# Kernel optimization log

Measured on AMD Instinct MI355X. Metric: run time of the kernel, lower is better.

Reference implementation:

```python
import jax, jax.numpy as jnp
import numpy as np

D_MODEL = 1024
STATE_DIM = 64
SEQ_L = 2048


def hippo_legs_A(N):
    n = jnp.arange(N, dtype=jnp.float32)
    two_n1 = 2.0 * n + 1.0
    sq = jnp.sqrt(two_n1[:, None] * two_n1[None, :])
    A = jnp.tril(sq, k=-1) * -1.0
    return A + jnp.diag(-(n + 1.0))


def setup_inputs() -> dict:
    key = jax.random.key(0)
    kB, kC = jax.random.split(key)
    N = STATE_DIM
    n = jnp.arange(N, dtype=jnp.float32)
    B_ref = jnp.sqrt(2.0 * n + 1.0)  # (N,)
    B = jnp.tile(B_ref[None, :], (D_MODEL, 1)) + 0.01 * jax.random.normal(kB, (D_MODEL, N), dtype=jnp.float32)
    C = 0.1 * jax.random.normal(kC, (D_MODEL, N), dtype=jnp.float32)
    D = jnp.zeros((D_MODEL,), dtype=jnp.float32)
    log_dt = jnp.log(jnp.asarray(0.1, dtype=jnp.float32))
    return {"B": B, "C": C, "D": D, "log_dt": log_dt, "L": SEQ_L}


def reference(B, C, D, log_dt, L):
    N = B.shape[1]
    A = hippo_legs_A(N)                       # (N,N) continuous-time HiPPO-LegS
    dt = jax.nn.softplus(log_dt) + 1e-06
    I = jnp.eye(N, dtype=A.dtype)
    lhs = I - 0.5 * dt * A
    rhs = I + 0.5 * dt * A
    A_bar = jnp.linalg.solve(lhs, rhs)        # (N,N) bilinear discretization
    B_bar = jnp.linalg.solve(lhs, (dt * B).T).T  # (d_model, N)
    A_bar_T = A_bar.T

    def step(x, _):
        y = jnp.sum(C * x, axis=-1)           # (d_model,)
        return x @ A_bar_T, y

    _, ys = jax.lax.scan(step, B_bar, None, length=L)  # ys: (L, d_model)
    K = ys.T                                   # (d_model, L)
    K = K.at[:, 0].add(D)
    return K[:, None, :]                       # (d_model, 1, L)
```

## Files before the change

kernel.cpp:

```cpp
#include <hip/hip_runtime.h>

typedef unsigned short ushort_t;
typedef unsigned int uint_t;
typedef short short8 __attribute__((ext_vector_type(8)));
typedef float f32x4 __attribute__((ext_vector_type(4)));

namespace {

template<int CTRL, int RM>
__device__ __forceinline__ float dpp_mov0(float v) {
  return __int_as_float(__builtin_amdgcn_update_dpp(
      0, __float_as_int(v), CTRL, RM, 0xF, false));
}
template<int CTRL, int RM>
__device__ __forceinline__ float dpp_mov1(float v) {
  return __int_as_float(__builtin_amdgcn_update_dpp(
      0x3f800000, __float_as_int(v), CTRL, RM, 0xF, false));
}

__device__ __forceinline__ float rl(float v, int k) {
  return __int_as_float(__builtin_amdgcn_readlane(__float_as_int(v), k));
}

struct Hoist {
  float cs0, cs1, cs2, cs3, cs4, cs5;
  float gs0, gs1, gs2, gs3, gs4, gs5;
  float r, inv_d, hr, alpha, k2;
};

__device__ __forceinline__ Hoist make_hoist(float dt, int n) {
  float h = 0.5f * dt, fn = (float)n;
  float r = sqrtf(2.f * fn + 1.f);
  float d = 1.f + h * (fn + 1.f);
  float inv_d = 1.f / d;
  float g = (1.f - h * fn) * inv_d;
  float c = g - 1.f;
  Hoist H;
  H.r = r; H.inv_d = inv_d; H.hr = h * r;
  H.alpha = 1.f + h * fn;
  H.k2 = r * (2.f - d) * inv_d;
#define COEF_STEP(IDX, CTRL, RM)                                        \
  H.cs##IDX = c; H.gs##IDX = g;                                         \
  { float cP = dpp_mov0<CTRL, RM>(c);                                   \
    float gP = dpp_mov1<CTRL, RM>(g);                                   \
    c = fmaf(g, cP, c); g = g * gP; }
  COEF_STEP(0, 0x111, 0xF)
  COEF_STEP(1, 0x112, 0xF)
  COEF_STEP(2, 0x114, 0xF)
  COEF_STEP(3, 0x118, 0xF)
  COEF_STEP(4, 0x142, 0xA)
  COEF_STEP(5, 0x143, 0xC)
#undef COEF_STEP
  return H;
}

__device__ __forceinline__ float abar_apply(float x, const Hoist& H) {
  float w1 = H.r * x, w2 = H.k2 * x;
#define APPLY_STEP(IDX, CTRL, RM)                                       \
  { float w1P = dpp_mov0<CTRL, RM>(w1);                                 \
    float w2P = dpp_mov0<CTRL, RM>(w2);                                 \
    w2 = fmaf(H.cs##IDX, w1P, fmaf(H.gs##IDX, w2P, w2));                \
    w1 += w1P; }
  APPLY_STEP(0, 0x111, 0xF)
  APPLY_STEP(1, 0x112, 0xF)
  APPLY_STEP(2, 0x114, 0xF)
  APPLY_STEP(3, 0x118, 0xF)
  APPLY_STEP(4, 0x142, 0xA)
  APPLY_STEP(5, 0x143, 0xC)
#undef APPLY_STEP
  float tp = dpp_mov0<0x138, 0xF>(w2);
  return H.inv_d * fmaf(-H.hr, w1 + tp, H.alpha * x);
}

template<int CTRL, int RM>
__device__ __forceinline__ void linrec_step(float& G, float& W) {
  float Wo = dpp_mov0<CTRL, RM>(W);
  float Go = dpp_mov1<CTRL, RM>(G);
  W = fmaf(G, Wo, W);
  G *= Go;
}
__device__ __forceinline__ float lhs_solve(float z, const Hoist& H) {
  float G = H.gs0, W = H.r * z * H.inv_d;
  linrec_step<0x111, 0xF>(G, W);
  linrec_step<0x112, 0xF>(G, W);
  linrec_step<0x114, 0xF>(G, W);
  linrec_step<0x118, 0xF>(G, W);
  linrec_step<0x142, 0xA>(G, W);
  linrec_step<0x143, 0xC>(G, W);
  float sp = dpp_mov0<0x138, 0xF>(W);
  return (z - H.hr * sp) * H.inv_d;
}

__device__ __forceinline__ float softplus_dt(float ldt) {
  return log1pf(expf(ldt)) + 1e-6f;
}

__device__ __forceinline__ void load_row_g(const float* __restrict__ base,
                                           float (&pc)[64]) {
  const float4* p4 = (const float4*)base;
  #pragma unroll
  for (int q = 0; q < 16; ++q) {
    float4 f = p4[q];
    pc[4*q+0] = f.x; pc[4*q+1] = f.y; pc[4*q+2] = f.z; pc[4*q+3] = f.w;
  }
}

__device__ __forceinline__ float qapply(const float (&pc)[64], float u) {
  float a0 = 0.f, a1 = 0.f, a2 = 0.f, a3 = 0.f;
  #pragma unroll
  for (int k = 0; k < 64; k += 4) {
    a0 = fmaf(pc[k + 0], rl(u, k + 0), a0);
    a1 = fmaf(pc[k + 1], rl(u, k + 1), a1);
    a2 = fmaf(pc[k + 2], rl(u, k + 2), a2);
    a3 = fmaf(pc[k + 3], rl(u, k + 3), a3);
  }
  return (a0 + a1) + (a2 + a3);
}

__device__ __forceinline__ float grow_matvec(const float* __restrict__ M,
                                             float u, int lane) {
  float a0 = 0.f, a1 = 0.f, a2 = 0.f, a3 = 0.f;
  const float4* m4 = (const float4*)(M + lane * 64);
  #pragma unroll
  for (int q = 0; q < 16; ++q) {
    float4 f = m4[q];
    a0 = fmaf(f.x, rl(u, 4 * q + 0), a0);
    a1 = fmaf(f.y, rl(u, 4 * q + 1), a1);
    a2 = fmaf(f.z, rl(u, 4 * q + 2), a2);
    a3 = fmaf(f.w, rl(u, 4 * q + 3), a3);
  }
  return (a0 + a1) + (a2 + a3);
}

__device__ __forceinline__ void split_store(float v, ushort_t* Hi,
                                            ushort_t* Lo, int row, int n) {
  uint_t uv = __float_as_uint(v);
  float hf = __uint_as_float(uv & 0xFFFF0000u);
  uint_t lv = __float_as_uint(v - hf);
  int idx = (row << 6) | (((n >> 3) ^ (row & 7)) << 3) | (n & 7);
  Hi[idx] = (ushort_t)(uv >> 16);
  Lo[idx] = (ushort_t)(lv >> 16);
}

__device__ __forceinline__ int frag_off(int row, int chunk) {
  return (row << 6) | ((chunk ^ (row & 7)) << 3);
}

}

__global__ __launch_bounds__(64) void hippo_pow(const float* __restrict__ ldt_p,
                                                float* __restrict__ A32c,
                                                float* __restrict__ QROW,
                                                float* __restrict__ Q2ROW) {
  const int lane = threadIdx.x;
  const int m = blockIdx.x;
  const float dt = softplus_dt(ldt_p[0]);
  const Hoist H = make_hoist(dt, lane);
  float x = (lane == m) ? 1.f : 0.f;
  #pragma unroll 1
  for (int s = 0; s < 32; ++s) x = abar_apply(x, H);
  A32c[lane * 64 + m] = x;
  #pragma unroll 1
  for (int s = 0; s < 32; ++s) x = abar_apply(x, H);
  QROW[m * 64 + lane] = x;
  #pragma unroll 1
  for (int s = 0; s < 64; ++s) x = abar_apply(x, H);
  Q2ROW[m * 64 + lane] = x;
}

__global__ __launch_bounds__(256, 2) void hippo_main(
    const float* __restrict__ B, const float* __restrict__ C,
    const float* __restrict__ Dv, const float* __restrict__ ldt_p,
    const float* __restrict__ A32c, const float* __restrict__ QROW,
    const float* __restrict__ Q2ROW, float* __restrict__ out) {
  __shared__ __align__(16) ushort_t Uh[32 * 64], Ulo[32 * 64];
  __shared__ __align__(16) ushort_t Vh[32 * 64], Vlo[32 * 64];
  const int d = blockIdx.x >> 1;
  const int h = blockIdx.x & 1;
  const int tau = threadIdx.x;
  const int lane = tau & 63;
  const int w = tau >> 6;
  const float dt = softplus_dt(ldt_p[0]);

  if (w == 0) {
    const Hoist H = make_hoist(dt, lane);
    float v = lhs_solve(dt * B[d * 64 + lane], H);
    if (h) v = grow_matvec(A32c, v, lane);
    #pragma unroll 1
    for (int j = 0; j < 32; ++j) {
      split_store(v, Vh, Vlo, j, lane);
      if (j < 31) v = abar_apply(v, H);
    }
  } else if (w == 1) {
    float pc[64];
    load_row_g(Q2ROW + lane * 64, pc);
    float u = C[d * 64 + lane];
    #pragma unroll 1
    for (int a = 0; a < 16; ++a) {
      split_store(u, Uh, Ulo, 2 * a, lane);
      if (a < 15) u = qapply(pc, u);
    }
  } else if (w == 2) {
    float pc[64];
    load_row_g(Q2ROW + lane * 64, pc);
    float u = grow_matvec(QROW, C[d * 64 + lane], lane);
    #pragma unroll 1
    for (int a = 0; a < 16; ++a) {
      split_store(u, Uh, Ulo, 2 * a + 1, lane);
      if (a < 15) u = qapply(pc, u);
    }
  }
  __syncthreads();

  const int it = w & 1;
  const int jt = w >> 1;
  const int arow = lane & 15;
  const int kg = lane >> 4;
  f32x4 acc = {0.f, 0.f, 0.f, 0.f};
  const int ia = (it << 4) + arow;
  const int jv = (jt << 4) + arow;
  #pragma unroll
  for (int k0 = 0; k0 < 2; ++k0) {
    const int ci = (k0 << 2) + kg;
    short8 ah = *(const short8*)&Uh[frag_off(ia, ci)];
    short8 al = *(const short8*)&Ulo[frag_off(ia, ci)];
    short8 bh = *(const short8*)&Vh[frag_off(jv, ci)];
    short8 bl = *(const short8*)&Vlo[frag_off(jv, ci)];
    acc = __builtin_amdgcn_mfma_f32_16x16x32_bf16(ah, bh, acc, 0, 0, 0);
    acc = __builtin_amdgcn_mfma_f32_16x16x32_bf16(al, bh, acc, 0, 0, 0);
    acc = __builtin_amdgcn_mfma_f32_16x16x32_bf16(ah, bl, acc, 0, 0, 0);
  }
  #pragma unroll
  for (int r = 0; r < 4; ++r) {
    const int i = (it << 4) + (kg << 2) + r;
    const int jg = (h << 5) + (jt << 4) + arow;
    float y = acc[r];
    if (i == 0 && jg == 0) y += Dv[d];
    out[((size_t)d << 11) + (i << 6) + jg] = y;
  }
}

extern "C" void kernel_launch(void* const* d_in, const int* in_sizes, int n_in,
                              void* d_out, int out_size, void* d_ws, size_t ws_size,
                              hipStream_t stream) {
  const float* B   = (const float*)d_in[0];
  const float* C   = (const float*)d_in[1];
  const float* Dv  = (const float*)d_in[2];
  const float* ldt = (const float*)d_in[3];
  const int d_model = in_sizes[2];
  float* A32c  = (float*)d_ws;
  float* QROW  = (float*)d_ws + 4096;
  float* Q2ROW = (float*)d_ws + 8192;
  hippo_pow<<<64, 64, 0, stream>>>(ldt, A32c, QROW, Q2ROW);
  hippo_main<<<2 * d_model, 256, 0, stream>>>(B, C, Dv, ldt, A32c, QROW, Q2ROW,
                                              (float*)d_out);
}
```

Measured before the change: 48.94 us.

## Split Krylov recurrence chains across more waves using precomputed matrix powers

Merges the two per-channel half-blocks into one 512-thread block where four waves each generate 16 state vectors (seeded via precomputed A^16/A^32/A^48) and four waves each generate 8 output-projection vectors stepping by A^256. A new small kernel precomputes the higher powers Q3/Q4. This shortens the serial dependent chains in the main kernel, at the cost of an extra launch, more matvec seeding work, and larger blocks with more LDS.

```diff
diff --git a/kernel.cpp b/kernel.cpp
--- a/kernel.cpp
+++ b/kernel.cpp
@@ -149,7 +149,9 @@
 }
 
 __global__ __launch_bounds__(64) void hippo_pow(const float* __restrict__ ldt_p,
-                                                float* __restrict__ A32c,
+                                                float* __restrict__ S16,
+                                                float* __restrict__ S32,
+                                                float* __restrict__ S48,
                                                 float* __restrict__ QROW,
                                                 float* __restrict__ Q2ROW) {
   const int lane = threadIdx.x;
@@ -158,56 +160,80 @@
   const Hoist H = make_hoist(dt, lane);
   float x = (lane == m) ? 1.f : 0.f;
   #pragma unroll 1
-  for (int s = 0; s < 32; ++s) x = abar_apply(x, H);
-  A32c[lane * 64 + m] = x;
-  #pragma unroll 1
-  for (int s = 0; s < 32; ++s) x = abar_apply(x, H);
+  for (int s = 0; s < 16; ++s) x = abar_apply(x, H);
+  S16[lane * 64 + m] = x;
+  #pragma unroll 1
+  for (int s = 0; s < 16; ++s) x = abar_apply(x, H);
+  S32[lane * 64 + m] = x;
+  #pragma unroll 1
+  for (int s = 0; s < 16; ++s) x = abar_apply(x, H);
+  S48[lane * 64 + m] = x;
+  #pragma unroll 1
+  for (int s = 0; s < 16; ++s) x = abar_apply(x, H);
   QROW[m * 64 + lane] = x;
   #pragma unroll 1
   for (int s = 0; s < 64; ++s) x = abar_apply(x, H);
   Q2ROW[m * 64 + lane] = x;
 }
 
-__global__ __launch_bounds__(256, 2) void hippo_main(
+__global__ __launch_bounds__(64) void hippo_qx(const float* __restrict__ QROW,
+                                               const float* __restrict__ Q2ROW,
+                                               float* __restrict__ Q3ROW,
+                                               float* __restrict__ Q4ROW) {
+  const int lane = threadIdx.x;
+  const int n = blockIdx.x;
+  const float u1 = QROW[n * 64 + lane];
+  const float u2 = Q2ROW[n * 64 + lane];
+  float a3 = 0.f, a4 = 0.f;
+  #pragma unroll 4
+  for (int p = 0; p < 64; ++p) {
+    float val = Q2ROW[p * 64 + lane];
+    a3 = fmaf(rl(u1, p), val, a3);
+    a4 = fmaf(rl(u2, p), val, a4);
+  }
+  Q3ROW[n * 64 + lane] = a3;
+  Q4ROW[n * 64 + lane] = a4;
+}
+
+__global__ __launch_bounds__(512, 2) void hippo_main(
     const float* __restrict__ B, const float* __restrict__ C,
     const float* __restrict__ Dv, const float* __restrict__ ldt_p,
-    const float* __restrict__ A32c, const float* __restrict__ QROW,
-    const float* __restrict__ Q2ROW, float* __restrict__ out) {
+    const float* __restrict__ S16, const float* __restrict__ S32,
+    const float* __restrict__ S48, const float* __restrict__ QROW,
+    const float* __restrict__ Q2ROW, const float* __restrict__ Q3ROW,
+    const float* __restrict__ Q4ROW, float* __restrict__ out) {
   __shared__ __align__(16) ushort_t Uh[32 * 64], Ulo[32 * 64];
-  __shared__ __align__(16) ushort_t Vh[32 * 64], Vlo[32 * 64];
-  const int d = blockIdx.x >> 1;
-  const int h = blockIdx.x & 1;
+  __shared__ __align__(16) ushort_t Vh[64 * 64], Vlo[64 * 64];
+  const int d = blockIdx.x;
   const int tau = threadIdx.x;
   const int lane = tau & 63;
   const int w = tau >> 6;
-  const float dt = softplus_dt(ldt_p[0]);
-
-  if (w == 0) {
+
+  if (w < 4) {
+    const float dt = softplus_dt(ldt_p[0]);
     const Hoist H = make_hoist(dt, lane);
     float v = lhs_solve(dt * B[d * 64 + lane], H);
-    if (h) v = grow_matvec(A32c, v, lane);
+    if (w == 1)      v = grow_matvec(S16, v, lane);
+    else if (w == 2) v = grow_matvec(S32, v, lane);
+    else if (w == 3) v = grow_matvec(S48, v, lane);
+    const int j0 = w << 4;
     #pragma unroll 1
-    for (int j = 0; j < 32; ++j) {
-      split_store(v, Vh, Vlo, j, lane);
-      if (j < 31) v = abar_apply(v, H);
+    for (int jj = 0; jj < 16; ++jj) {
+      split_store(v, Vh, Vlo, j0 + jj, lane);
+      if (jj < 15) v = abar_apply(v, H);
     }
-  } else if (w == 1) {
+  } else {
+    const int i0 = w - 4;
+    float u = C[d * 64 + lane];
+    if (i0 == 1)      u = grow_matvec(QROW, u, lane);
+    else if (i0 == 2) u = grow_matvec(Q2ROW, u, lane);
+    else if (i0 == 3) u = grow_matvec(Q3ROW, u, lane);
     float pc[64];
-    load_row_g(Q2ROW + lane * 64, pc);
-    float u = C[d * 64 + lane];
+    load_row_g(Q4ROW + lane * 64, pc);
     #pragma unroll 1
-    for (int a = 0; a < 16; ++a) {
-      split_store(u, Uh, Ulo, 2 * a, lane);
-      if (a < 15) u = qapply(pc, u);
-    }
-  } else if (w == 2) {
-    float pc[64];
-    load_row_g(Q2ROW + lane * 64, pc);
-    float u = grow_matvec(QROW, C[d * 64 + lane], lane);
-    #pragma unroll 1
-    for (int a = 0; a < 16; ++a) {
-      split_store(u, Uh, Ulo, 2 * a + 1, lane);
-      if (a < 15) u = qapply(pc, u);
+    for (int a = 0; a < 8; ++a) {
+      split_store(u, Uh, Ulo, i0 + (a << 2), lane);
+      if (a < 7) u = qapply(pc, u);
     }
   }
   __syncthreads();
@@ -233,7 +259,7 @@
   #pragma unroll
   for (int r = 0; r < 4; ++r) {
     const int i = (it << 4) + (kg << 2) + r;
-    const int jg = (h << 5) + (jt << 4) + arow;
+    const int jg = (jt << 4) + arow;
     float y = acc[r];
     if (i == 0 && jg == 0) y += Dv[d];
     out[((size_t)d << 11) + (i << 6) + jg] = y;
@@ -248,10 +274,16 @@
   const float* Dv  = (const float*)d_in[2];
   const float* ldt = (const float*)d_in[3];
   const int d_model = in_sizes[2];
-  float* A32c  = (float*)d_ws;
-  float* QROW  = (float*)d_ws + 4096;
-  float* Q2ROW = (float*)d_ws + 8192;
-  hippo_pow<<<64, 64, 0, stream>>>(ldt, A32c, QROW, Q2ROW);
-  hippo_main<<<2 * d_model, 256, 0, stream>>>(B, C, Dv, ldt, A32c, QROW, Q2ROW,
-                                              (float*)d_out);
-}
+  float* S16   = (float*)d_ws;
+  float* S32   = (float*)d_ws + 4096;
+  float* S48   = (float*)d_ws + 8192;
+  float* QROW  = (float*)d_ws + 12288;
+  float* Q2ROW = (float*)d_ws + 16384;
+  float* Q3ROW = (float*)d_ws + 20480;
+  float* Q4ROW = (float*)d_ws + 24576;
+  hippo_pow<<<64, 64, 0, stream>>>(ldt, S16, S32, S48, QROW, Q2ROW);
+  hippo_qx<<<64, 64, 0, stream>>>(QROW, Q2ROW, Q3ROW, Q4ROW);
+  hippo_main<<<d_model, 512, 0, stream>>>(B, C, Dv, ldt, S16, S32, S48,
+                                          QROW, Q2ROW, Q3ROW, Q4ROW,
+                                          (float*)d_out);
+}
```

New measurement: 48.97 us. About the same (+0.1%).
